# Kernel optimization log

Hardware: AMD Instinct MI355X
Metric: run time of the kernel (lower is better)

Reference implementation:

```python
import jax, jax.numpy as jnp
import numpy as np
from jax import lax

# Quantization / conv config (mirrors QuantizedConv2d init args)
INPUT_ZP = -3
OUTPUT_ZP = 5
INPUT_SCALE = 0.05
OUTPUT_SCALE = 0.1
STRIDE = 1
PAD = (1, 1)   # (pad_h, pad_w)
DILATION = 1
GROUPS = 1
FEATURE_BITWIDTH = 8
QMIN = -(1 << (FEATURE_BITWIDTH - 1))          # -128
QMAX = (1 << (FEATURE_BITWIDTH - 1)) - 1       # 127

N, CIN, H, W = 32, 128, 56, 56
COUT, KH, KW = 256, 3, 3


def setup_inputs() -> dict:
    key = jax.random.key(0)
    k1, k2, k3, k4 = jax.random.split(key, 4)
    # int8-range quantized input / weight (stored as int32 arrays)
    x = jax.random.randint(k1, (N, CIN, H, W), 0, 256, dtype=jnp.int32) - 128
    weight = jax.random.randint(k2, (COUT, CIN, KH, KW), 0, 128, dtype=jnp.int32) - 64
    bias = jax.random.randint(k3, (COUT,), -32, 32, dtype=jnp.int32)
    # per-output-channel weight scale, shape [COUT,1,1] so it broadcasts over NCHW
    weight_scale = jax.random.uniform(k4, (COUT, 1, 1), dtype=jnp.float32) * 0.01 + 1e-4
    return {"x": x, "weight": weight, "bias": bias, "weight_scale": weight_scale}


def reference(x, weight, bias, weight_scale):
    ph, pw = PAD
    # Pad with the input zero point (quantized-domain padding)
    x_f = jnp.pad(x.astype(jnp.float32), ((0, 0), (0, 0), (ph, ph), (pw, pw)),
                  constant_values=float(INPUT_ZP))
    w_f = weight.astype(jnp.float32)
    b_f = bias.astype(jnp.float32)[None, :, None, None]
    # float32 conv (GPU path of the original), padding already applied
    acc = lax.conv_general_dilated(
        x_f, w_f,
        window_strides=(STRIDE, STRIDE),
        padding='VALID',
        rhs_dilation=(DILATION, DILATION),
        feature_group_count=GROUPS,
        dimension_numbers=('NCHW', 'OIHW', 'NCHW'))
    # original: conv2d(..., bias=q_bias) then round -> int32, then bias added AGAIN
    out = jnp.round(acc + b_f).astype(jnp.int32)
    out = out + bias[None, :, None, None]
    # dequant -> requant epilogue with per-channel weight scale
    out = (out.astype(jnp.float32) * INPUT_SCALE * weight_scale[None]
           / OUTPUT_SCALE + OUTPUT_ZP)
    out = jnp.clip(jnp.round(out), QMIN, QMAX).astype(jnp.int8)
    return out
```

## Files before the change

### kernel.cpp

```cpp
#include <hip/hip_runtime.h>


typedef __attribute__((ext_vector_type(4))) int i32x4;

#define NB_N 32
#define CIN 128
#define HH 56
#define WW 56
#define PH 58
#define COUT 256
#define PIX_PER_IMG (HH*WW)
#define X_IMG_INTS (PIX_PER_IMG*CIN)
#define XP_ROW_BYTES (PH*CIN)
#define XP_IMG_BYTES (PH*XP_ROW_BYTES)
#define XQ_PAD_BYTES ((size_t)NB_N*XP_IMG_BYTES)
#define A4_BYTES (4*XP_ROW_BYTES)

#define WPR 33
__global__ __launch_bounds__(256) void pack_x_kernel(const int* __restrict__ x,
                                                     signed char* __restrict__ xq) {
    __shared__ int tile[WW * WPR];
    int nh = blockIdx.x;
    int n = nh / HH, h = nh - n * HH;
    const int* src = x + (size_t)n * X_IMG_INTS + h * WW;
    signed char* img = xq + (size_t)n * XP_IMG_BYTES;
    int q = threadIdx.x & 15;
    int cg4 = threadIdx.x >> 4;
    if (q < 14) {
#pragma unroll
        for (int i = 0; i < 2; ++i) {
            int cg = cg4 + i * 16;
            i32x4 v0 = *(const i32x4*)(src + (cg * 4 + 0) * PIX_PER_IMG + q * 4);
            i32x4 v1 = *(const i32x4*)(src + (cg * 4 + 1) * PIX_PER_IMG + q * 4);
            i32x4 v2 = *(const i32x4*)(src + (cg * 4 + 2) * PIX_PER_IMG + q * 4);
            i32x4 v3 = *(const i32x4*)(src + (cg * 4 + 3) * PIX_PER_IMG + q * 4);
#pragma unroll
            for (int j = 0; j < 4; ++j) {
                int word = (v0[j] & 255) | ((v1[j] & 255) << 8) |
                           ((v2[j] & 255) << 16) | (v3[j] << 24);
                tile[(q * 4 + j) * WPR + cg] = word;
            }
        }
    }
    const i32x4 pad = {(int)0xFDFDFDFD, (int)0xFDFDFDFD, (int)0xFDFDFDFD, (int)0xFDFDFDFD};
    {
        int t = threadIdx.x;
        if (t < 16) {
            int w = (t >> 3) ? 57 : 0;
            *(i32x4*)(img + ((size_t)(h + 1) * PH + w) * CIN + (t & 7) * 16) = pad;
        }
    }
    if (h == 0) {
        for (int t = threadIdx.x; t < 464; t += 256)
            *(i32x4*)(img + (size_t)t * 16) = pad;
    }
    if (h == HH - 1) {
        for (int t = threadIdx.x; t < 464; t += 256)
            *(i32x4*)(img + (size_t)57 * XP_ROW_BYTES + t * 16) = pad;
    }
    __syncthreads();
    int* dst = (int*)(img + ((size_t)(h + 1) * PH + 1) * CIN);
#pragma unroll
    for (int i = 0; i < 7; ++i) {
        int t = i * 256 + threadIdx.x;
        int w = t >> 5, c4 = t & 31;
        dst[w * 32 + c4] = tile[w * WPR + c4];
    }
}

__global__ __launch_bounds__(256) void pack_w_kernel(const int* __restrict__ w,
                                                     signed char* __restrict__ wq) {
    int idx = blockIdx.x * 256 + threadIdx.x;
    if (idx >= 9 * 2 * 16 * 64) return;
    int lane = idx & 63;
    int fid = idx >> 6;
    int t = fid / 32;
    int rem = fid - t * 32;
    int kb = rem >> 4;
    int nf = rem & 15;
    int cout = nf * 16 + (lane & 15);
    int cinb = kb * 64 + (lane >> 4) * 16;
    int kh = t / 3, kw = t - kh * 3;
    union { signed char b[16]; i32x4 v; } u;
#pragma unroll
    for (int j = 0; j < 16; ++j) {
        int cin = cinb + j;
        u.b[j] = (signed char)w[((cout * CIN + cin) * 3 + kh) * 3 + kw];
    }
    *(i32x4*)(wq + (size_t)idx * 16) = u.v;
}

__global__ __launch_bounds__(512) void conv_kernel(const signed char* __restrict__ xq,
                                                   const signed char* __restrict__ wq,
                                                   const int* __restrict__ bias,
                                                   const float* __restrict__ wscale,
                                                   int* __restrict__ out) {
    __shared__ __align__(16) signed char lds[A4_BYTES];
    const int tid = threadIdx.x;
    const int lane = tid & 63, wv = tid >> 6;
    const int row = lane & 15, grp = lane >> 4;

    int orig = (blockIdx.x & 7) * 112 + (blockIdx.x >> 3);
    int n = orig / 28;
    int rb = orig - n * 28;

    const signed char* ximg = xq + (size_t)n * XP_IMG_BYTES + (size_t)rb * 2 * XP_ROW_BYTES;

#pragma unroll
    for (int k = 0; k < 4; ++k) {
        int d = k * 8192 + tid * 16;
        if (d < A4_BYTES) {
            int g = d ^ (((d >> 7) & 7) << 4);
            i32x4 v = *(const i32x4*)(ximg + g);
            *(i32x4*)(lds + d) = v;
        }
    }

    float sc[2];
    int b2[2];
    const int coutbase = wv * 32;
#pragma unroll
    for (int j = 0; j < 2; ++j) {
        int cout = coutbase + j * 16 + row;
        sc[j] = wscale[cout] * 0.5f;
        b2[j] = 2 * bias[cout];
    }

    __syncthreads();

    int pc[7];
#pragma unroll
    for (int m = 0; m < 7; ++m) {
        int off = m * 16 + row;
        int lr = (off >= 56);
        int w = off - lr * 56;
        pc[m] = (lr + 1) * PH + (w + 1);
    }

    const int tapd[9] = {-PH - 1, -PH, -PH + 1, -1, 0, 1, PH - 1, PH, PH + 1};

    const signed char* wbase = wq + (size_t)(wv * 2) * 1024 + lane * 16;

    i32x4 acc[7][2] = {};
    i32x4 bn0 = *(const i32x4*)(wbase);
    i32x4 bn1 = *(const i32x4*)(wbase + 1024);

#pragma unroll
    for (int s = 0; s < 18; ++s) {
        const int t = s >> 1, kb = s & 1;
        i32x4 b0 = bn0, b1 = bn1;
        if (s < 17) {
            bn0 = *(const i32x4*)(wbase + (s + 1) * 16384);
            bn1 = *(const i32x4*)(wbase + (s + 1) * 16384 + 1024);
        }
        i32x4 a[7];
#pragma unroll
        for (int m = 0; m < 7; ++m) {
            int pix = pc[m] + tapd[t];
            int g = (pix << 7) + (kb << 6) + (grp << 4);
            int d = g ^ ((pix & 7) << 4);
            a[m] = *(const i32x4*)(lds + d);
        }
#pragma unroll
        for (int m = 0; m < 7; ++m) {
            acc[m][0] = __builtin_amdgcn_mfma_i32_16x16x64_i8(a[m], b0, acc[m][0], 0, 0, 0);
            acc[m][1] = __builtin_amdgcn_mfma_i32_16x16x64_i8(a[m], b1, acc[m][1], 0, 0, 0);
        }
    }

    const int pixbase = rb * 112;
#pragma unroll
    for (int m = 0; m < 7; ++m) {
        int pl = pixbase + m * 16 + grp * 4;
        size_t obase = (size_t)n * (COUT * PIX_PER_IMG) + pl;
#pragma unroll
        for (int j = 0; j < 2; ++j) {
            int cout = coutbase + j * 16 + row;
            i32x4 v;
#pragma unroll
            for (int r = 0; r < 4; ++r) {
                int o = acc[m][j][r] + b2[j];
                float f = fmaf((float)o, sc[j], 5.0f);
                f = rintf(f);
                f = fminf(fmaxf(f, -128.0f), 127.0f);
                v[r] = (int)f;
            }
            *(i32x4*)(out + obase + (size_t)cout * PIX_PER_IMG) = v;
        }
    }
}

extern "C" void kernel_launch(void* const* d_in, const int* in_sizes, int n_in,
                              void* d_out, int out_size, void* d_ws, size_t ws_size,
                              hipStream_t stream) {
    const int* x = (const int*)d_in[0];
    const int* w = (const int*)d_in[1];
    const int* bias = (const int*)d_in[2];
    const float* ws = (const float*)d_in[3];
    int* out = (int*)d_out;

    signed char* xq = (signed char*)d_ws;
    signed char* wq = xq + XQ_PAD_BYTES;

    pack_x_kernel<<<NB_N * HH, 256, 0, stream>>>(x, xq);
    pack_w_kernel<<<72, 256, 0, stream>>>(w, wq);
    conv_kernel<<<896, 512, 0, stream>>>(xq, wq, bias, ws, out);
}
```

Baseline: 68.97 us.

## Switch conv to 32x32x32 int8 MFMA with 64-pixel tiles and 4-wave blocks

Replaces the 16x16x64 int8 MFMA tiling (112 pixels per block, 8 waves, each wave handling 32 output channels) with 32x32x32 MFMA over 64-pixel tiles. Each block now has 4 waves covering 64 output channels apiece, and the grid grows to 1568 blocks. The weight packing is reorganized for the new B-operand layout, and weight prefetch becomes double-buffered two steps ahead. Block tiles now start in the middle of rows, so they can straddle two image rows; the LDS stage still copies 4 padded rows. The larger MFMA shape is meant to raise arithmetic density per LDS read, at the cost of more LDS fetches per output and a different occupancy profile.

```diff
diff --git a/kernel.cpp b/kernel.cpp
--- a/kernel.cpp
+++ b/kernel.cpp
@@ -2,6 +2,7 @@
 
 
 typedef __attribute__((ext_vector_type(4))) int i32x4;
+typedef __attribute__((ext_vector_type(16))) int i32x16;
 
 #define NB_N 32
 #define CIN 128
@@ -71,15 +72,14 @@
 __global__ __launch_bounds__(256) void pack_w_kernel(const int* __restrict__ w,
                                                      signed char* __restrict__ wq) {
     int idx = blockIdx.x * 256 + threadIdx.x;
-    if (idx >= 9 * 2 * 16 * 64) return;
+    if (idx >= 9 * 4 * 8 * 64) return;
     int lane = idx & 63;
     int fid = idx >> 6;
-    int t = fid / 32;
-    int rem = fid - t * 32;
-    int kb = rem >> 4;
-    int nf = rem & 15;
-    int cout = nf * 16 + (lane & 15);
-    int cinb = kb * 64 + (lane >> 4) * 16;
+    int nf = fid & 7;
+    int kblk = (fid >> 3) & 3;
+    int t = fid >> 5;
+    int cout = nf * 32 + (lane & 31);
+    int cinb = kblk * 32 + (lane >> 5) * 16;
     int kh = t / 3, kw = t - kh * 3;
     union { signed char b[16]; i32x4 v; } u;
 #pragma unroll
@@ -90,7 +90,7 @@
     *(i32x4*)(wq + (size_t)idx * 16) = u.v;
 }
 
-__global__ __launch_bounds__(512) void conv_kernel(const signed char* __restrict__ xq,
+__global__ __launch_bounds__(256) void conv_kernel(const signed char* __restrict__ xq,
                                                    const signed char* __restrict__ wq,
                                                    const int* __restrict__ bias,
                                                    const float* __restrict__ wscale,
@@ -98,17 +98,20 @@
     __shared__ __align__(16) signed char lds[A4_BYTES];
     const int tid = threadIdx.x;
     const int lane = tid & 63, wv = tid >> 6;
-    const int row = lane & 15, grp = lane >> 4;
-
-    int orig = (blockIdx.x & 7) * 112 + (blockIdx.x >> 3);
-    int n = orig / 28;
-    int rb = orig - n * 28;
-
-    const signed char* ximg = xq + (size_t)n * XP_IMG_BYTES + (size_t)rb * 2 * XP_ROW_BYTES;
-
-#pragma unroll
-    for (int k = 0; k < 4; ++k) {
-        int d = k * 8192 + tid * 16;
+    const int col32 = lane & 31, khalf = lane >> 5;
+
+    int orig = (blockIdx.x & 7) * 196 + (blockIdx.x >> 3);
+    int n = orig / 49;
+    int b = orig - n * 49;
+    const int pb = b * 64;
+    const int r0 = pb / 56;
+    const int cbase = pb - r0 * 56;
+
+    const signed char* ximg = xq + (size_t)n * XP_IMG_BYTES + (size_t)r0 * XP_ROW_BYTES;
+
+#pragma unroll
+    for (int k = 0; k < 8; ++k) {
+        int d = k * 4096 + tid * 16;
         if (d < A4_BYTES) {
             int g = d ^ (((d >> 7) & 7) << 4);
             i32x4 v = *(const i32x4*)(ximg + g);
@@ -118,74 +121,77 @@
 
     float sc[2];
     int b2[2];
-    const int coutbase = wv * 32;
-#pragma unroll
-    for (int j = 0; j < 2; ++j) {
-        int cout = coutbase + j * 16 + row;
-        sc[j] = wscale[cout] * 0.5f;
-        b2[j] = 2 * bias[cout];
+#pragma unroll
+    for (int nn = 0; nn < 2; ++nn) {
+        int cout = wv * 64 + nn * 32 + col32;
+        sc[nn] = wscale[cout] * 0.5f;
+        b2[nn] = 2 * bias[cout];
     }
 
     __syncthreads();
 
-    int pc[7];
-#pragma unroll
-    for (int m = 0; m < 7; ++m) {
-        int off = m * 16 + row;
-        int lr = (off >= 56);
-        int w = off - lr * 56;
-        pc[m] = (lr + 1) * PH + (w + 1);
+    int pm[2];
+#pragma unroll
+    for (int m = 0; m < 2; ++m) {
+        int co = cbase + m * 32 + col32;
+        int lr = (co >= 56);
+        int c = co - lr * 56;
+        pm[m] = (lr + 1) * PH + (c + 1);
     }
 
     const int tapd[9] = {-PH - 1, -PH, -PH + 1, -1, 0, 1, PH - 1, PH, PH + 1};
 
     const signed char* wbase = wq + (size_t)(wv * 2) * 1024 + lane * 16;
 
-    i32x4 acc[7][2] = {};
-    i32x4 bn0 = *(const i32x4*)(wbase);
-    i32x4 bn1 = *(const i32x4*)(wbase + 1024);
-
-#pragma unroll
-    for (int s = 0; s < 18; ++s) {
-        const int t = s >> 1, kb = s & 1;
-        i32x4 b0 = bn0, b1 = bn1;
-        if (s < 17) {
-            bn0 = *(const i32x4*)(wbase + (s + 1) * 16384);
-            bn1 = *(const i32x4*)(wbase + (s + 1) * 16384 + 1024);
-        }
-        i32x4 a[7];
-#pragma unroll
-        for (int m = 0; m < 7; ++m) {
-            int pix = pc[m] + tapd[t];
-            int g = (pix << 7) + (kb << 6) + (grp << 4);
+    i32x16 acc[2][2] = {};
+    i32x4 bn[2][2];
+    bn[0][0] = *(const i32x4*)(wbase);
+    bn[0][1] = *(const i32x4*)(wbase + 1024);
+    bn[1][0] = *(const i32x4*)(wbase + 8192);
+    bn[1][1] = *(const i32x4*)(wbase + 8192 + 1024);
+
+#pragma unroll
+    for (int s = 0; s < 36; ++s) {
+        const int t = s >> 2, kblk = s & 3;
+        i32x4 a[2];
+#pragma unroll
+        for (int m = 0; m < 2; ++m) {
+            int pix = pm[m] + tapd[t];
+            int g = (pix << 7) + (kblk << 5) + (khalf << 4);
             int d = g ^ ((pix & 7) << 4);
             a[m] = *(const i32x4*)(lds + d);
         }
-#pragma unroll
-        for (int m = 0; m < 7; ++m) {
-            acc[m][0] = __builtin_amdgcn_mfma_i32_16x16x64_i8(a[m], b0, acc[m][0], 0, 0, 0);
-            acc[m][1] = __builtin_amdgcn_mfma_i32_16x16x64_i8(a[m], b1, acc[m][1], 0, 0, 0);
-        }
-    }
-
-    const int pixbase = rb * 112;
-#pragma unroll
-    for (int m = 0; m < 7; ++m) {
-        int pl = pixbase + m * 16 + grp * 4;
-        size_t obase = (size_t)n * (COUT * PIX_PER_IMG) + pl;
-#pragma unroll
-        for (int j = 0; j < 2; ++j) {
-            int cout = coutbase + j * 16 + row;
-            i32x4 v;
-#pragma unroll
-            for (int r = 0; r < 4; ++r) {
-                int o = acc[m][j][r] + b2[j];
-                float f = fmaf((float)o, sc[j], 5.0f);
-                f = rintf(f);
-                f = fminf(fmaxf(f, -128.0f), 127.0f);
-                v[r] = (int)f;
+        i32x4 b0 = bn[s & 1][0], b1 = bn[s & 1][1];
+        acc[0][0] = __builtin_amdgcn_mfma_i32_32x32x32_i8(a[0], b0, acc[0][0], 0, 0, 0);
+        acc[0][1] = __builtin_amdgcn_mfma_i32_32x32x32_i8(a[0], b1, acc[0][1], 0, 0, 0);
+        acc[1][0] = __builtin_amdgcn_mfma_i32_32x32x32_i8(a[1], b0, acc[1][0], 0, 0, 0);
+        acc[1][1] = __builtin_amdgcn_mfma_i32_32x32x32_i8(a[1], b1, acc[1][1], 0, 0, 0);
+        if (s < 34) {
+            bn[s & 1][0] = *(const i32x4*)(wbase + (size_t)(s + 2) * 8192);
+            bn[s & 1][1] = *(const i32x4*)(wbase + (size_t)(s + 2) * 8192 + 1024);
+        }
+    }
+
+    const size_t nbase = (size_t)n * (COUT * PIX_PER_IMG);
+#pragma unroll
+    for (int m = 0; m < 2; ++m) {
+#pragma unroll
+        for (int nn = 0; nn < 2; ++nn) {
+            int cout = wv * 64 + nn * 32 + col32;
+            size_t obase = nbase + (size_t)cout * PIX_PER_IMG + pb + m * 32 + 4 * khalf;
+#pragma unroll
+            for (int q = 0; q < 4; ++q) {
+                i32x4 v;
+#pragma unroll
+                for (int r = 0; r < 4; ++r) {
+                    int o = acc[m][nn][q * 4 + r] + b2[nn];
+                    float f = fmaf((float)o, sc[nn], 5.0f);
+                    f = rintf(f);
+                    f = fminf(fmaxf(f, -128.0f), 127.0f);
+                    v[r] = (int)f;
+                }
+                *(i32x4*)(out + obase + q * 8) = v;
             }
-            *(i32x4*)(out + obase + (size_t)cout * PIX_PER_IMG) = v;
         }
     }
 }
@@ -204,5 +210,5 @@
 
     pack_x_kernel<<<NB_N * HH, 256, 0, stream>>>(x, xq);
     pack_w_kernel<<<72, 256, 0, stream>>>(w, wq);
-    conv_kernel<<<896, 512, 0, stream>>>(xq, wq, bias, ws, out);
-}
+    conv_kernel<<<1568, 256, 0, stream>>>(xq, wq, bias, ws, out);
+}
```

Result: no change. 69.04 us (+0.1%).

## Fuse input int8 packing into conv kernel, drop separate pack_x pass

Applied to the files above, without the earlier changes.

Removes the standalone pack_x kernel and has each conv block read its four padded input rows directly from the int32 NCHW input. The block converts them to int8 and writes them into swizzled LDS, filling zero-point padding in place. This cuts one kernel launch and the round trip through the packed int8 workspace. The cost is that halo rows are now read twice by adjacent blocks as int32, which is four times the bytes of int8. The LDS stores are also narrower 4-byte scalar writes, which may conflict on banks.

```diff
diff --git a/kernel.cpp b/kernel.cpp
--- a/kernel.cpp
+++ b/kernel.cpp
@@ -12,61 +12,7 @@
 #define PIX_PER_IMG (HH*WW)
 #define X_IMG_INTS (PIX_PER_IMG*CIN)
 #define XP_ROW_BYTES (PH*CIN)
-#define XP_IMG_BYTES (PH*XP_ROW_BYTES)
-#define XQ_PAD_BYTES ((size_t)NB_N*XP_IMG_BYTES)
 #define A4_BYTES (4*XP_ROW_BYTES)
-
-#define WPR 33
-__global__ __launch_bounds__(256) void pack_x_kernel(const int* __restrict__ x,
-                                                     signed char* __restrict__ xq) {
-    __shared__ int tile[WW * WPR];
-    int nh = blockIdx.x;
-    int n = nh / HH, h = nh - n * HH;
-    const int* src = x + (size_t)n * X_IMG_INTS + h * WW;
-    signed char* img = xq + (size_t)n * XP_IMG_BYTES;
-    int q = threadIdx.x & 15;
-    int cg4 = threadIdx.x >> 4;
-    if (q < 14) {
-#pragma unroll
-        for (int i = 0; i < 2; ++i) {
-            int cg = cg4 + i * 16;
-            i32x4 v0 = *(const i32x4*)(src + (cg * 4 + 0) * PIX_PER_IMG + q * 4);
-            i32x4 v1 = *(const i32x4*)(src + (cg * 4 + 1) * PIX_PER_IMG + q * 4);
-            i32x4 v2 = *(const i32x4*)(src + (cg * 4 + 2) * PIX_PER_IMG + q * 4);
-            i32x4 v3 = *(const i32x4*)(src + (cg * 4 + 3) * PIX_PER_IMG + q * 4);
-#pragma unroll
-            for (int j = 0; j < 4; ++j) {
-                int word = (v0[j] & 255) | ((v1[j] & 255) << 8) |
-                           ((v2[j] & 255) << 16) | (v3[j] << 24);
-                tile[(q * 4 + j) * WPR + cg] = word;
-            }
-        }
-    }
-    const i32x4 pad = {(int)0xFDFDFDFD, (int)0xFDFDFDFD, (int)0xFDFDFDFD, (int)0xFDFDFDFD};
-    {
-        int t = threadIdx.x;
-        if (t < 16) {
-            int w = (t >> 3) ? 57 : 0;
-            *(i32x4*)(img + ((size_t)(h + 1) * PH + w) * CIN + (t & 7) * 16) = pad;
-        }
-    }
-    if (h == 0) {
-        for (int t = threadIdx.x; t < 464; t += 256)
-            *(i32x4*)(img + (size_t)t * 16) = pad;
-    }
-    if (h == HH - 1) {
-        for (int t = threadIdx.x; t < 464; t += 256)
-            *(i32x4*)(img + (size_t)57 * XP_ROW_BYTES + t * 16) = pad;
-    }
-    __syncthreads();
-    int* dst = (int*)(img + ((size_t)(h + 1) * PH + 1) * CIN);
-#pragma unroll
-    for (int i = 0; i < 7; ++i) {
-        int t = i * 256 + threadIdx.x;
-        int w = t >> 5, c4 = t & 31;
-        dst[w * 32 + c4] = tile[w * WPR + c4];
-    }
-}
 
 __global__ __launch_bounds__(256) void pack_w_kernel(const int* __restrict__ w,
                                                      signed char* __restrict__ wq) {
@@ -90,7 +36,7 @@
     *(i32x4*)(wq + (size_t)idx * 16) = u.v;
 }
 
-__global__ __launch_bounds__(512) void conv_kernel(const signed char* __restrict__ xq,
+__global__ __launch_bounds__(512) void conv_kernel(const int* __restrict__ x,
                                                    const signed char* __restrict__ wq,
                                                    const int* __restrict__ bias,
                                                    const float* __restrict__ wscale,
@@ -104,15 +50,44 @@
     int n = orig / 28;
     int rb = orig - n * 28;
 
-    const signed char* ximg = xq + (size_t)n * XP_IMG_BYTES + (size_t)rb * 2 * XP_ROW_BYTES;
-
+    {
+        const i32x4 padv = {(int)0xFDFDFDFD, (int)0xFDFDFDFD, (int)0xFDFDFDFD, (int)0xFDFDFDFD};
+        int srow = tid >> 7;
+        int cq = (tid >> 2) & 31;
+        int wseg = tid & 3;
+        int h = rb * 2 - 1 + srow;
+        if ((unsigned)h < (unsigned)HH) {
+            const int* src0 = x + ((size_t)n * CIN + cq * 4) * PIX_PER_IMG + h * WW;
 #pragma unroll
-    for (int k = 0; k < 4; ++k) {
-        int d = k * 8192 + tid * 16;
-        if (d < A4_BYTES) {
-            int g = d ^ (((d >> 7) & 7) << 4);
-            i32x4 v = *(const i32x4*)(ximg + g);
-            *(i32x4*)(lds + d) = v;
+            for (int qi = 0; qi < 4; ++qi) {
+                int q = wseg + qi * 4;
+                if (q < 14) {
+                    i32x4 v0 = *(const i32x4*)(src0 + 0 * PIX_PER_IMG + q * 4);
+                    i32x4 v1 = *(const i32x4*)(src0 + 1 * PIX_PER_IMG + q * 4);
+                    i32x4 v2 = *(const i32x4*)(src0 + 2 * PIX_PER_IMG + q * 4);
+                    i32x4 v3 = *(const i32x4*)(src0 + 3 * PIX_PER_IMG + q * 4);
+#pragma unroll
+                    for (int j = 0; j < 4; ++j) {
+                        int word = (v0[j] & 255) | ((v1[j] & 255) << 8) |
+                                   ((v2[j] & 255) << 16) | (v3[j] << 24);
+                        int pix = srow * PH + q * 4 + j + 1;
+                        int d = ((pix << 7) + cq * 4) ^ ((pix & 7) << 4);
+                        *(int*)(lds + d) = word;
+                    }
+                }
+            }
+            if (wseg < 2 && cq < 8) {
+                int pix = srow * PH + (wseg ? 57 : 0);
+                int d = ((pix << 7) + cq * 16) ^ ((pix & 7) << 4);
+                *(i32x4*)(lds + d) = padv;
+            }
+        } else {
+            for (int u = (tid & 127); u < 464; u += 128) {
+                int g = srow * XP_ROW_BYTES + u * 16;
+                int pix = g >> 7;
+                int d = g ^ ((pix & 7) << 4);
+                *(i32x4*)(lds + d) = padv;
+            }
         }
     }
 
@@ -199,10 +174,8 @@
     const float* ws = (const float*)d_in[3];
     int* out = (int*)d_out;
 
-    signed char* xq = (signed char*)d_ws;
-    signed char* wq = xq + XQ_PAD_BYTES;
+    signed char* wq = (signed char*)d_ws;
 
-    pack_x_kernel<<<NB_N * HH, 256, 0, stream>>>(x, xq);
     pack_w_kernel<<<72, 256, 0, stream>>>(w, wq);
-    conv_kernel<<<896, 512, 0, stream>>>(xq, wq, bias, ws, out);
+    conv_kernel<<<896, 512, 0, stream>>>(x, wq, bias, ws, out);
 }
```

Result: faster. 66.70 us (-3.3%).
